# Kernel tuning notes

Hardware: AMD Instinct MI355X
Metric: run time of the kernel (lower is better)

The kernel has to match this reference:

```python
import jax, jax.numpy as jnp
import numpy as np

K = 3          # up_kernel
S = 2          # scale_factor
C_IN = 256
C_COMP = 64
C_ENC = K * K * 1 * S * S  # up_kernel^2 * up_group * scale^2 = 36


def conv2d(x, w, b, pad):
    y = jax.lax.conv_general_dilated(
        x, w, window_strides=(1, 1), padding=[(pad, pad), (pad, pad)],
        dimension_numbers=('NCHW', 'OIHW', 'NCHW'))
    return y + b[None, :, None, None]


def extract_patches(x, k):
    # x: [B,C,H,W] -> [B,C,k*k,H,W], row-major kernel order (matches F.unfold)
    B, C, H, W = x.shape
    p = k // 2
    xp = jnp.pad(x, ((0, 0), (0, 0), (p, p), (p, p)))
    sl = [xp[:, :, i:i + H, j:j + W] for i in range(k) for j in range(k)]
    return jnp.stack(sl, axis=2)


def setup_inputs() -> dict:
    key = jax.random.key(0)
    k1, k2, k3 = jax.random.split(key, 3)
    B, H, W = 8, 64, 64
    x = jax.random.normal(k1, (B, C_IN, H, W), dtype=jnp.float32)
    # channel_compressor: 1x1 conv, xavier-uniform
    lim1 = float(np.sqrt(6.0 / (C_IN + C_COMP)))
    w1 = jax.random.uniform(k2, (C_COMP, C_IN, 1, 1), minval=-lim1, maxval=lim1, dtype=jnp.float32)
    b1 = jnp.zeros((C_COMP,), jnp.float32)
    # content_encoder: 3x3 conv, normal(std=0.001)
    w2 = 0.001 * jax.random.normal(k3, (C_ENC, C_COMP, 3, 3), dtype=jnp.float32)
    b2 = jnp.zeros((C_ENC,), jnp.float32)
    return {'x': x, 'w1': w1, 'b1': b1, 'w2': w2, 'b2': b2}


def reference(x, w1, b1, w2, b2):
    B, C, H, W = x.shape
    # gradient guidance from channel mean
    mean = jnp.mean(x, axis=1, keepdims=True)                 # [B,1,H,W]
    mpatch = extract_patches(mean, K)[:, 0]                   # [B,K^2,H,W]
    grad = mpatch - mean[:, 0][:, None]                       # [B,K^2,H,W]
    grad = 1.0 / (grad * grad + 0.2)
    # dynamic kernel prediction
    comp = conv2d(x, w1, b1, pad=0)                           # [B,64,H,W]
    kern = conv2d(comp, w2, b2, pad=1)                        # [B,K^2*S^2,H,W]
    kern = kern.reshape(B, K * K, S * S, H, W)
    m = grad[:, :, None] * kern                               # [B,K^2,S^2,H,W]
    # pixel_shuffle(upscale=S) on the S^2 channel dim, then squeeze:
    # m[b,kk,p*S+q,h,w] -> mask[b,kk,h*S+p,w*S+q]
    m = m.reshape(B, K * K, S, S, H, W).transpose(0, 1, 4, 2, 5, 3)  # [B,K^2,H,S,W,S]
    m = jax.nn.softmax(m, axis=1)
    # CARAFE reassembly: out[b,c,h*S+p,w*S+q] = sum_kk patches[b,c,kk,h,w]*m[b,kk,h,p,w,q]
    patches = extract_patches(x, K)                           # [B,C,K^2,H,W]
    out = jnp.einsum('bckhw,bkhpwq->bchpwq', patches, m)
    return out.reshape(B, C, H * S, W * S)
```

## Files before the change

kernel.cpp:

```cpp
#include <hip/hip_runtime.h>


#define W1BF_OFF  0
#define MEAN_OFF  8192
#define W2B_OFF   40960
#define CPP_OFF   54784

typedef __attribute__((ext_vector_type(8))) short bf8;
typedef __attribute__((ext_vector_type(8))) unsigned short us8;
typedef __attribute__((ext_vector_type(4))) float f4;
typedef __attribute__((ext_vector_type(2))) float f2;

static __device__ inline unsigned short f2bf(float f) {
    unsigned u = __float_as_uint(f);
    unsigned r = u + 0x7FFFu + ((u >> 16) & 1u);
    return (unsigned short)(r >> 16);
}

__global__ __launch_bounds__(256) void k_init(const float* __restrict__ w1,
                                              const float* __restrict__ w2,
                                              float* __restrict__ ws) {
    int bid = blockIdx.x, t = threadIdx.x;
    if (bid < 65) {
        int id = bid * 256 + t;
        if (id < 16640) {
            int px = id >> 3, part = id & 7;
            int b = px / 260, r = px % 260;
            int y, xx;
            if (r < 66)       { y = 0;  xx = r; }
            else if (r < 132) { y = 65; xx = r - 66; }
            else              { int s = r - 132; y = (s & 63) + 1; xx = (s >> 6) ? 65 : 0; }
            uint4* p = (uint4*)((unsigned short*)(ws + CPP_OFF)
                                + ((size_t)(b * 66 + y) * 66 + xx) * 64) + part;
            *p = uint4{0, 0, 0, 0};
        }
        return;
    }
    unsigned short* w1bf = (unsigned short*)(ws + W1BF_OFF);
    unsigned short* w2b  = (unsigned short*)(ws + W2B_OFF);
    int gid = (bid - 65) * 256 + t;
    int stride = 68 * 256;
    for (int i = gid; i < 64 * 256; i += stride)
        w1bf[i] = f2bf(w1[i]);
    for (int i = gid; i < 48 * 576; i += stride) {
        int o = i / 576, k = i % 576;
        int s = k >> 6, j = k & 63;
        w2b[i] = (o < 36) ? f2bf(w2[o * 576 + j * 9 + s]) : (unsigned short)0;
    }
}

__global__ __launch_bounds__(256) void k_comp(const float* __restrict__ x,
                                              const float* __restrict__ b1,
                                              float* __restrict__ ws) {
    const unsigned short* w1bf = (const unsigned short*)(ws + W1BF_OFF);
    float* mean = ws + MEAN_OFF;
    unsigned short* cpp = (unsigned short*)(ws + CPP_OFF);
    __shared__ unsigned short xbf[64][260];
    __shared__ float msp[16][64];
    __shared__ float ctile[64][68];

    int bid = blockIdx.x;
    int swz = (bid & 7) * 64 + (bid >> 3);
    int b = swz >> 6, h = swz & 63;
    int t = threadIdx.x;

    int cg = t >> 4;
    int px4 = (t & 15) * 4;
    float ms0 = 0.f, ms1 = 0.f, ms2 = 0.f, ms3 = 0.f;
    const float* xb = x + (size_t)b * 256 * 4096 + h * 64;
#pragma unroll
    for (int it = 0; it < 16; it++) {
        int c = it * 16 + cg;
        f4 v = *(const f4*)(xb + (size_t)c * 4096 + px4);
        ms0 += v[0]; ms1 += v[1]; ms2 += v[2]; ms3 += v[3];
        xbf[px4 + 0][c] = f2bf(v[0]);
        xbf[px4 + 1][c] = f2bf(v[1]);
        xbf[px4 + 2][c] = f2bf(v[2]);
        xbf[px4 + 3][c] = f2bf(v[3]);
    }
    msp[cg][px4 + 0] = ms0; msp[cg][px4 + 1] = ms1;
    msp[cg][px4 + 2] = ms2; msp[cg][px4 + 3] = ms3;
    __syncthreads();
    if (t < 64) {
        float s = 0.f;
#pragma unroll
        for (int k2 = 0; k2 < 16; k2++) s += msp[k2][t];
        mean[(b * 64 + h) * 64 + t] = s * (1.f / 256.f);
    }

    int wid = __builtin_amdgcn_readfirstlane(t >> 6);
    int l = t & 63, lm = l & 15, lk = l >> 4;
    bf8 bfrag[8];
    const unsigned short* wp = w1bf + (size_t)(wid * 16 + lm) * 256 + lk * 8;
#pragma unroll
    for (int ks = 0; ks < 8; ks++) bfrag[ks] = *(const bf8*)(wp + ks * 32);
    float bb = b1[wid * 16 + lm];
#pragma unroll
    for (int mt = 0; mt < 4; mt++) {
        f4 acc = {bb, bb, bb, bb};
#pragma unroll
        for (int ks = 0; ks < 8; ks++) {
            bf8 af = *(const bf8*)(&xbf[mt * 16 + lm][ks * 32 + lk * 8]);
            acc = __builtin_amdgcn_mfma_f32_16x16x32_bf16(af, bfrag[ks], acc, 0, 0, 0);
        }
#pragma unroll
        for (int r = 0; r < 4; r++)
            ctile[mt * 16 + lk * 4 + r][wid * 16 + lm] = acc[r];
    }
    __syncthreads();

    int px = t >> 2, jq = t & 3;
    us8 o0, o1;
#pragma unroll
    for (int i = 0; i < 8; i++) {
        o0[i] = f2bf(ctile[px][jq * 16 + i]);
        o1[i] = f2bf(ctile[px][jq * 16 + 8 + i]);
    }
    unsigned short* dst = cpp + ((size_t)(b * 66 + h + 1) * 66 + (px + 1)) * 64 + jq * 16;
    *(us8*)dst = o0;
    *(us8*)(dst + 8) = o1;
}

__global__ __launch_bounds__(384) void k_fused(const float* __restrict__ x,
                                               const float* __restrict__ b2,
                                               const float* __restrict__ ws,
                                               float* __restrict__ out) {
    const unsigned short* w2b = (const unsigned short*)(ws + W2B_OFF);
    const unsigned short* cpp = (const unsigned short*)(ws + CPP_OFF);
    const float* mean = ws + MEAN_OFF;
    __shared__ float kern[64][49];
    __shared__ float msk[64][37];

    int bid = blockIdx.x;
    int swz = (bid & 7) * 64 + (bid >> 3);
    int b = swz >> 6, h = swz & 63;
    int t = threadIdx.x;
    int wid = __builtin_amdgcn_readfirstlane(t >> 6);
    int l = t & 63;

    {
        int o = wid % 3, ph = wid / 3;
        int lm = l & 15, lk = l >> 4;
        bf8 bfrag[18];
        const unsigned short* bp = w2b + (size_t)(o * 16 + lm) * 576 + lk * 8;
#pragma unroll
        for (int ks = 0; ks < 18; ks++) bfrag[ks] = *(const bf8*)(bp + ks * 32);

        const unsigned short* abase = cpp + ((size_t)(b * 66 + h) * 66 + lm) * 64 + lk * 8;
#pragma unroll
        for (int hf = 0; hf < 2; hf++) {
            int w0 = (ph * 2 + hf) * 16;
            const unsigned short* ab = abase + w0 * 64;
            f4 acc = {0.f, 0.f, 0.f, 0.f};
#pragma unroll
            for (int ks = 0; ks < 18; ks++) {
                const int s = ks >> 1, jh = ks & 1;
                const int dy = s / 3, dx = s % 3;
                bf8 af = *(const bf8*)(ab + (dy * 66 + dx) * 64 + jh * 32);
                acc = __builtin_amdgcn_mfma_f32_16x16x32_bf16(af, bfrag[ks], acc, 0, 0, 0);
            }
#pragma unroll
            for (int r = 0; r < 4; r++)
                kern[w0 + lk * 4 + r][o * 16 + lm] = acc[r];
        }
    }
    __syncthreads();

    if (t < 256) {
        int w = t & 63, pq = t >> 6;
        float mc = mean[(b * 64 + h) * 64 + w];
        float v[9], mx = -1e30f;
#pragma unroll
        for (int kk = 0; kk < 9; kk++) {
            int y = h + kk / 3 - 1, xw = w + kk % 3 - 1;
            float mv = ((unsigned)y < 64u && (unsigned)xw < 64u)
                           ? mean[(b * 64 + y) * 64 + xw] : 0.f;
            float d = mv - mc;
            float g = 1.f / (d * d + 0.2f);
            v[kk] = g * (kern[w][kk * 4 + pq] + b2[kk * 4 + pq]);
            mx = fmaxf(mx, v[kk]);
        }
        float s = 0.f;
#pragma unroll
        for (int kk = 0; kk < 9; kk++) { v[kk] = __expf(v[kk] - mx); s += v[kk]; }
        float inv = 1.f / s;
#pragma unroll
        for (int kk = 0; kk < 9; kk++) msk[w][pq * 9 + kk] = v[kk] * inv;
    }
    __syncthreads();

    int wv = t >> 6;
    int w = l;

    float m[4][9];
#pragma unroll
    for (int pq = 0; pq < 4; pq++)
#pragma unroll
        for (int kk = 0; kk < 9; kk++) m[pq][kk] = msk[w][pq * 9 + kk];

    for (int c = wv; c < 256; c += 6) {
        const float* xb = x + (size_t)(b * 256 + c) * 4096;
        float p[3][3];
#pragma unroll
        for (int dy = 0; dy < 3; dy++) {
            int y = h + dy - 1;
            bool yok = (unsigned)y < 64u;
#pragma unroll
            for (int dx = 0; dx < 3; dx++) {
                int xx = w + dx - 1;
                p[dy][dx] = (yok && (unsigned)xx < 64u) ? xb[y * 64 + xx] : 0.f;
            }
        }
        float o00 = 0.f, o01 = 0.f, o10 = 0.f, o11 = 0.f;
#pragma unroll
        for (int kk = 0; kk < 9; kk++) {
            float pv = p[kk / 3][kk % 3];
            o00 += pv * m[0][kk];
            o01 += pv * m[1][kk];
            o10 += pv * m[2][kk];
            o11 += pv * m[3][kk];
        }
        float* ob = out + ((size_t)(b * 256 + c) * 128 + 2 * h) * 128 + 2 * w;
        *(f2*)ob = f2{o00, o01};
        *(f2*)(ob + 128) = f2{o10, o11};
    }
}

extern "C" void kernel_launch(void* const* d_in, const int* in_sizes, int n_in,
                              void* d_out, int out_size, void* d_ws, size_t ws_size,
                              hipStream_t stream) {
    const float* x  = (const float*)d_in[0];
    const float* w1 = (const float*)d_in[1];
    const float* b1 = (const float*)d_in[2];
    const float* w2 = (const float*)d_in[3];
    const float* b2 = (const float*)d_in[4];
    float* out = (float*)d_out;
    float* ws  = (float*)d_ws;

    k_init<<<133, 256, 0, stream>>>(w1, w2, ws);
    k_comp<<<512, 256, 0, stream>>>(x, b1, ws);
    k_fused<<<512, 384, 0, stream>>>(x, b2, ws, out);
}
```

Baseline: 67.72 us.

## Split fused mask/reassembly kernel into mask kernel and wider output kernel

The fused kernel is split in two. One kernel computes the softmax masks and writes them to a workspace buffer in global memory. A second kernel launches 2048 blocks, each covering a quarter of the channels for one row, and runs the reassembly. This spreads the bandwidth-bound output stage over more blocks and occupancy than the 512-block fused kernel, at the cost of an extra launch and a global round trip for the mask, which each channel-group block reads again.

```diff
diff --git a/kernel.cpp b/kernel.cpp
--- a/kernel.cpp
+++ b/kernel.cpp
@@ -4,7 +4,8 @@
 #define W1BF_OFF  0
 #define MEAN_OFF  8192
 #define W2B_OFF   40960
-#define CPP_OFF   54784
+#define MASK_OFF  54784
+#define CPP_OFF   1234432
 
 typedef __attribute__((ext_vector_type(8))) short bf8;
 typedef __attribute__((ext_vector_type(8))) unsigned short us8;
@@ -121,15 +122,14 @@
     *(us8*)(dst + 8) = o1;
 }
 
-__global__ __launch_bounds__(384) void k_fused(const float* __restrict__ x,
-                                               const float* __restrict__ b2,
-                                               const float* __restrict__ ws,
-                                               float* __restrict__ out) {
+__global__ __launch_bounds__(384) void k_mask(const float* __restrict__ b2,
+                                              float* __restrict__ ws) {
     const unsigned short* w2b = (const unsigned short*)(ws + W2B_OFF);
     const unsigned short* cpp = (const unsigned short*)(ws + CPP_OFF);
     const float* mean = ws + MEAN_OFF;
+    float* mask = ws + MASK_OFF;
     __shared__ float kern[64][49];
-    __shared__ float msk[64][37];
+    __shared__ float msk2[64 * 36];
 
     int bid = blockIdx.x;
     int swz = (bid & 7) * 64 + (bid >> 3);
@@ -185,20 +185,35 @@
         for (int kk = 0; kk < 9; kk++) { v[kk] = __expf(v[kk] - mx); s += v[kk]; }
         float inv = 1.f / s;
 #pragma unroll
-        for (int kk = 0; kk < 9; kk++) msk[w][pq * 9 + kk] = v[kk] * inv;
-    }
-    __syncthreads();
-
-    int wv = t >> 6;
-    int w = l;
-
+        for (int kk = 0; kk < 9; kk++) msk2[w * 36 + pq * 9 + kk] = v[kk] * inv;
+    }
+    __syncthreads();
+
+    float* mgbl = mask + (size_t)((b * 64 + h) * 64) * 36;
+    for (int i = t; i < 576; i += 384)
+        ((f4*)mgbl)[i] = ((const f4*)msk2)[i];
+}
+
+__global__ __launch_bounds__(256) void k_out(const float* __restrict__ x,
+                                             const float* __restrict__ ws,
+                                             float* __restrict__ out) {
+    const float* mask = ws + MASK_OFF;
+    int bid = blockIdx.x;
+    int swz = (bid & 7) * 256 + (bid >> 3);
+    int b = swz >> 8;
+    int rem = swz & 255;
+    int h = rem >> 2, cg = rem & 3;
+    int t = threadIdx.x;
+    int w = t & 63, cs = t >> 6;
+
+    const float* mrow = mask + (size_t)(((b * 64 + h) * 64 + w)) * 36;
     float m[4][9];
 #pragma unroll
     for (int pq = 0; pq < 4; pq++)
 #pragma unroll
-        for (int kk = 0; kk < 9; kk++) m[pq][kk] = msk[w][pq * 9 + kk];
-
-    for (int c = wv; c < 256; c += 6) {
+        for (int kk = 0; kk < 9; kk++) m[pq][kk] = mrow[pq * 9 + kk];
+
+    for (int c = cg * 64 + cs; c < cg * 64 + 64; c += 4) {
         const float* xb = x + (size_t)(b * 256 + c) * 4096;
         float p[3][3];
 #pragma unroll
@@ -239,5 +254,6 @@
 
     k_init<<<133, 256, 0, stream>>>(w1, w2, ws);
     k_comp<<<512, 256, 0, stream>>>(x, b1, ws);
-    k_fused<<<512, 384, 0, stream>>>(x, b2, ws, out);
-}
+    k_mask<<<512, 384, 0, stream>>>(b2, ws);
+    k_out<<<2048, 256, 0, stream>>>(x, ws, out);
+}
```

Measured after the change: 72.67 us. 7.3% more time.
